# Optimization experiments

Hardware: AMD Instinct MI355X
Metric: run time of the kernel (lower is better)

The kernel has to match this reference:

```python
import jax, jax.numpy as jnp
import numpy as np

OUT = 7  # out_size


def setup_inputs() -> dict:
    key = jax.random.key(0)
    kx, k1, k2, k3, k4 = jax.random.split(key, 5)
    B, C, H, W, Q = 4, 256, 128, 128, 100
    x = jax.random.normal(kx, (B, C, H, W), dtype=jnp.float32)
    # valid boxes: start in [0, W/2), extent in [8, W/2) -> always in-bounds, nonempty
    x1 = jax.random.randint(k1, (B, Q), 0, W // 2)
    y1 = jax.random.randint(k2, (B, Q), 0, H // 2)
    x2 = x1 + jax.random.randint(k3, (B, Q), 8, W // 2)
    y2 = y1 + jax.random.randint(k4, (B, Q), 8, H // 2)
    bidx = jnp.broadcast_to(jnp.arange(B, dtype=jnp.int32)[:, None], (B, Q))
    rois = jnp.stack([bidx, x1, y1, x2, y2], axis=-1).astype(jnp.int32)
    return {"x": x, "rois": rois}


def _bin_edges(start, length, nbins):
    # adaptive_avg_pool2d bin boundaries for bin k over a region of given length:
    #   lo_k = floor(k*L/n), hi_k = ceil((k+1)*L/n)
    # start, length: [B,Q] int; returns (starts, ends) each [B,Q,nbins]
    k = jnp.arange(nbins)
    lo = start[..., None] + (k * length[..., None]) // nbins
    hi = start[..., None] - ((-(k + 1) * length[..., None]) // nbins)  # ceil div
    return lo, hi


def reference(x, rois):
    # x: [B,C,H,W] float, rois: [B,Q,5] int (batch_idx, x1, y1, x2, y2)
    B, C, H, W = x.shape
    Q = rois.shape[1]
    oh = ow = OUT
    # Summed-area table S[b, y, x, c] = sum of x over rows < y, cols < x.
    xc = jnp.moveaxis(x, 1, -1)                       # [B,H,W,C]
    S = jnp.cumsum(jnp.cumsum(xc, axis=1), axis=2)
    S = jnp.pad(S, ((0, 0), (1, 0), (1, 0), (0, 0)))  # [B,H+1,W+1,C]

    x1, y1, x2, y2 = rois[..., 1], rois[..., 2], rois[..., 3], rois[..., 4]
    ys, ye = _bin_edges(y1, y2 - y1, oh)              # [B,Q,oh]
    xs, xe = _bin_edges(x1, x2 - x1, ow)              # [B,Q,ow]

    b = jnp.arange(B)[:, None, None, None]            # [B,1,1,1]
    Ys, Ye = ys[:, :, :, None], ye[:, :, :, None]     # [B,Q,oh,1]
    Xs, Xe = xs[:, :, None, :], xe[:, :, None, :]     # [B,Q,1,ow]

    # rectangle sums per bin via SAT corner differences -> [B,Q,oh,ow,C]
    sums = S[b, Ye, Xe] - S[b, Ys, Xe] - S[b, Ye, Xs] + S[b, Ys, Xs]
    area = ((Ye - Ys) * (Xe - Xs)).astype(x.dtype)[..., None]
    out = sums / area                                  # bin averages

    out = jnp.moveaxis(out, -1, 2)                     # [B,Q,C,oh,ow]
    return out.reshape(B, Q * C, oh, ow)               # cat ROIs along channel dim
```

## Files before the change

### kernel.cpp

```cpp
#include <hip/hip_runtime.h>

#define B_ 4
#define C_ 256
#define H_ 128
#define W_ 128
#define Q_ 100

__global__ __launch_bounds__(256) void roipool_kernel(const float4* __restrict__ x4,
                                                      const int* __restrict__ rois,
                                                      float* __restrict__ out) {
    __shared__ float sat[H_ * W_];

    const int c   = blockIdx.x & 255;
    const int b   = blockIdx.x >> 8;
    const int tid = threadIdx.x;

    const float4* src = x4 + (size_t)(b * C_ + c) * (H_ * W_ / 4);
    float4* s4 = (float4*)sat;
    #pragma unroll
    for (int i = 0; i < 16; ++i)
        s4[i * 256 + tid] = src[i * 256 + tid];
    __syncthreads();

    const int wave = tid >> 6, lane = tid & 63;
    for (int r = wave; r < H_; r += 4) {
        float v0 = sat[r * W_ + 2 * lane];
        float v1 = sat[r * W_ + 2 * lane + 1];
        float s  = v0 + v1;
        #pragma unroll
        for (int d = 1; d < 64; d <<= 1) {
            float t = __shfl_up(s, d);
            if (lane >= d) s += t;
        }
        float excl = s - (v0 + v1);
        sat[r * W_ + 2 * lane]     = excl + v0;
        sat[r * W_ + 2 * lane + 1] = excl + v0 + v1;
    }
    __syncthreads();

    if (tid < W_) {
        float acc = 0.f;
        #pragma unroll 8
        for (int y = 0; y < H_; ++y) {
            acc += sat[y * W_ + tid];
            sat[y * W_ + tid] = acc;
        }
    }
    __syncthreads();

    const int* rb = rois + (size_t)b * Q_ * 5;
    for (int t = tid; t < Q_ * 49; t += 256) {
        const int q   = t / 49;
        const int bin = t - q * 49;
        const int oy  = bin / 7;
        const int ox  = bin - oy * 7;

        const int x1 = rb[q * 5 + 1];
        const int y1 = rb[q * 5 + 2];
        const int Lx = rb[q * 5 + 3] - x1;
        const int Ly = rb[q * 5 + 4] - y1;

        const int ys = y1 + (oy * Ly) / 7;
        const int ye = y1 + ((oy + 1) * Ly + 6) / 7;
        const int xs = x1 + (ox * Lx) / 7;
        const int xe = x1 + ((ox + 1) * Lx + 6) / 7;

        const float s11 = sat[(ye - 1) * W_ + (xe - 1)];
        const float s01 = (ys > 0) ? sat[(ys - 1) * W_ + (xe - 1)] : 0.f;
        const float s10 = (xs > 0) ? sat[(ye - 1) * W_ + (xs - 1)] : 0.f;
        const float s00 = (ys > 0 && xs > 0) ? sat[(ys - 1) * W_ + (xs - 1)] : 0.f;

        const float area = (float)((ye - ys) * (xe - xs));
        out[(((size_t)(b * Q_ + q)) * C_ + c) * 49 + bin] =
            (s11 - s01 - s10 + s00) / area;
    }
}

extern "C" void kernel_launch(void* const* d_in, const int* in_sizes, int n_in,
                              void* d_out, int out_size, void* d_ws, size_t ws_size,
                              hipStream_t stream) {
    const float* x    = (const float*)d_in[0];
    const int*   rois = (const int*)d_in[1];
    float*       outp = (float*)d_out;

    roipool_kernel<<<B_ * C_, 256, 0, stream>>>((const float4*)x, rois, outp);
}
```

Before: 131.1 us.

## Parallelize SAT column scan across 512 threads with padded shared rows

Doubles the block size to 512 threads and pads shared-memory rows to 132 floats. The column prefix sum, which previously ran serially over 128 rows using only 128 threads, is split into four 32-row segments scanned in parallel. A small carry table then adds each segment's offset back in a parallel fix-up pass. The aim is to remove the serial column-scan bottleneck and use more threads per channel, at the cost of extra barriers, more shared memory (which may lower occupancy), and one more full pass over shared memory.

```diff
diff --git a/kernel.cpp b/kernel.cpp
--- a/kernel.cpp
+++ b/kernel.cpp
@@ -5,11 +5,13 @@
 #define H_ 128
 #define W_ 128
 #define Q_ 100
+#define WP_ 132
 
-__global__ __launch_bounds__(256) void roipool_kernel(const float4* __restrict__ x4,
-                                                      const int* __restrict__ rois,
-                                                      float* __restrict__ out) {
-    __shared__ float sat[H_ * W_];
+__global__ __launch_bounds__(512, 4) void roipool_kernel(const float4* __restrict__ x4,
+                                                         const int* __restrict__ rois,
+                                                         float* __restrict__ out) {
+    __shared__ float sat[H_ * WP_];
+    __shared__ float qt[4][W_];
 
     const int c   = blockIdx.x & 255;
     const int b   = blockIdx.x >> 8;
@@ -18,38 +20,63 @@
     const float4* src = x4 + (size_t)(b * C_ + c) * (H_ * W_ / 4);
     float4* s4 = (float4*)sat;
     #pragma unroll
-    for (int i = 0; i < 16; ++i)
-        s4[i * 256 + tid] = src[i * 256 + tid];
+    for (int i = 0; i < 8; ++i) {
+        int idx  = i * 512 + tid;
+        int row  = idx >> 5;
+        int col4 = idx & 31;
+        s4[row * (WP_ / 4) + col4] = src[idx];
+    }
     __syncthreads();
 
     const int wave = tid >> 6, lane = tid & 63;
-    for (int r = wave; r < H_; r += 4) {
-        float v0 = sat[r * W_ + 2 * lane];
-        float v1 = sat[r * W_ + 2 * lane + 1];
-        float s  = v0 + v1;
+    for (int r = wave; r < H_; r += 8) {
+        float2* p2 = (float2*)(sat + r * WP_);
+        float2 v = p2[lane];
+        float s  = v.x + v.y;
         #pragma unroll
         for (int d = 1; d < 64; d <<= 1) {
             float t = __shfl_up(s, d);
             if (lane >= d) s += t;
         }
-        float excl = s - (v0 + v1);
-        sat[r * W_ + 2 * lane]     = excl + v0;
-        sat[r * W_ + 2 * lane + 1] = excl + v0 + v1;
+        float excl = s - (v.x + v.y);
+        p2[lane] = make_float2(excl + v.x, excl + v.x + v.y);
+    }
+    __syncthreads();
+
+    {
+        const int qy = tid >> 7;
+        const int x  = tid & 127;
+        float acc = 0.f;
+        #pragma unroll
+        for (int j = 0; j < 32; ++j) {
+            const int y = qy * 32 + j;
+            acc += sat[y * WP_ + x];
+            sat[y * WP_ + x] = acc;
+        }
+        qt[qy][x] = acc;
     }
     __syncthreads();
 
     if (tid < W_) {
-        float acc = 0.f;
-        #pragma unroll 8
-        for (int y = 0; y < H_; ++y) {
-            acc += sat[y * W_ + tid];
-            sat[y * W_ + tid] = acc;
-        }
+        const int x = tid;
+        float t0 = qt[0][x], t1 = qt[1][x], t2 = qt[2][x];
+        qt[1][x] = t0;
+        qt[2][x] = t0 + t1;
+        qt[3][x] = t0 + t1 + t2;
+    }
+    __syncthreads();
+
+    #pragma unroll
+    for (int j = 0; j < 24; ++j) {
+        const int e = j * 512 + tid;
+        const int y = 32 + (e >> 7);
+        const int x = e & 127;
+        sat[y * WP_ + x] += qt[y >> 5][x];
     }
     __syncthreads();
 
     const int* rb = rois + (size_t)b * Q_ * 5;
-    for (int t = tid; t < Q_ * 49; t += 256) {
+    for (int t = tid; t < Q_ * 49; t += 512) {
         const int q   = t / 49;
         const int bin = t - q * 49;
         const int oy  = bin / 7;
@@ -65,10 +92,10 @@
         const int xs = x1 + (ox * Lx) / 7;
         const int xe = x1 + ((ox + 1) * Lx + 6) / 7;
 
-        const float s11 = sat[(ye - 1) * W_ + (xe - 1)];
-        const float s01 = (ys > 0) ? sat[(ys - 1) * W_ + (xe - 1)] : 0.f;
-        const float s10 = (xs > 0) ? sat[(ye - 1) * W_ + (xs - 1)] : 0.f;
-        const float s00 = (ys > 0 && xs > 0) ? sat[(ys - 1) * W_ + (xs - 1)] : 0.f;
+        const float s11 = sat[(ye - 1) * WP_ + (xe - 1)];
+        const float s01 = (ys > 0) ? sat[(ys - 1) * WP_ + (xe - 1)] : 0.f;
+        const float s10 = (xs > 0) ? sat[(ye - 1) * WP_ + (xs - 1)] : 0.f;
+        const float s00 = (ys > 0 && xs > 0) ? sat[(ys - 1) * WP_ + (xs - 1)] : 0.f;
 
         const float area = (float)((ye - ys) * (xe - xs));
         out[(((size_t)(b * Q_ + q)) * C_ + c) * 49 + bin] =
@@ -83,5 +110,5 @@
     const int*   rois = (const int*)d_in[1];
     float*       outp = (float*)d_out;
 
-    roipool_kernel<<<B_ * C_, 256, 0, stream>>>((const float4*)x, rois, outp);
+    roipool_kernel<<<B_ * C_, 512, 0, stream>>>((const float4*)x, rois, outp);
 }
```

Result: faster. 118.8 us (-9.4%).
